# Performance work log

Hardware: AMD Instinct MI355X
Metric: run time of the kernel (lower is better)

## Reference

```python
import jax, jax.numpy as jnp
import numpy as np

B, T, C, H = 2, 2048, 1024, 16
D = C // H  # head_dim = 64


def setup_inputs() -> dict:
    key = jax.random.key(0)
    k1, k2, k3 = jax.random.split(key, 3)
    scale = 0.02
    return {
        "x": jax.random.normal(k1, (B, T, C), dtype=jnp.float32),
        "w_qkv": jax.random.normal(k2, (C, 3 * C), dtype=jnp.float32) * scale,
        "b_qkv": jnp.zeros((3 * C,), dtype=jnp.float32),
        "w_out": jax.random.normal(k3, (C, C), dtype=jnp.float32) * scale,
        "b_out": jnp.zeros((C,), dtype=jnp.float32),
    }


def reference(x, w_qkv, b_qkv, w_out, b_out):
    b, t, c = x.shape
    qkv = x @ w_qkv + b_qkv                       # [b, t, 3c]
    q, k, v = jnp.split(qkv, 3, axis=-1)
    # [b, t, c] -> [b, h, t, d]
    q = q.reshape(b, t, H, D).transpose(0, 2, 1, 3)
    k = k.reshape(b, t, H, D).transpose(0, 2, 1, 3)
    v = v.reshape(b, t, H, D).transpose(0, 2, 1, 3)
    scores = jnp.einsum("bhqd,bhkd->bhqk", q, k) / jnp.sqrt(jnp.asarray(D, dtype=q.dtype))
    causal = jnp.tril(jnp.ones((t, t), dtype=bool))
    scores = jnp.where(causal, scores, jnp.finfo(scores.dtype).min)
    attn = jax.nn.softmax(scores, axis=-1)        # [b, h, q, k]
    out = jnp.einsum("bhqk,bhkd->bhqd", attn, v)  # [b, h, t, d]
    out = out.transpose(0, 2, 1, 3).reshape(b, t, c)
    return out @ w_out + b_out
```

## Files before the change

### kernel.cpp

```cpp
#include <hip/hip_runtime.h>

#define B_ 2
#define T_ 2048
#define C_ 1024
#define H_ 16
#define D_ 64

using bf16x8 = __attribute__((ext_vector_type(8))) short;
using f32x4  = __attribute__((ext_vector_type(4))) float;

static __device__ __forceinline__ short f2bf(float f) {
  unsigned u = __builtin_bit_cast(unsigned, f);
  unsigned r = u + 0x7fffu + ((u >> 16) & 1u);
  return (short)(r >> 16);
}

#define GLD16(gp, lp) __builtin_amdgcn_global_load_lds( \
    (const __attribute__((address_space(1))) void*)(gp), \
    (__attribute__((address_space(3))) void*)(lp), 16, 0, 0)

__global__ __launch_bounds__(256) void cast_f32_bf16(const float* __restrict__ in,
                                                     short* __restrict__ out) {
  int i = blockIdx.x * blockDim.x + threadIdx.x;
  float4 v = ((const float4*)in)[i];
  short4 o;
  o.x = f2bf(v.x); o.y = f2bf(v.y); o.z = f2bf(v.z); o.w = f2bf(v.w);
  ((short4*)out)[i] = o;
}

__global__ __launch_bounds__(256) void transpose_cast(const float* __restrict__ in,
                                                      short* __restrict__ out,
                                                      int R, int N) {
  __shared__ float tile[32][33];
  int bx = blockIdx.x * 32, by = blockIdx.y * 32;
  int tx = threadIdx.x, ty = threadIdx.y;
  #pragma unroll
  for (int j = 0; j < 32; j += 8)
    tile[ty + j][tx] = in[(size_t)(by + ty + j) * N + bx + tx];
  __syncthreads();
  #pragma unroll
  for (int j = 0; j < 32; j += 8)
    out[(size_t)(bx + ty + j) * R + by + tx] = f2bf(tile[tx][ty + j]);
}

__global__ __launch_bounds__(256) void gemm_qkv(const short* __restrict__ A,
                                                const short* __restrict__ Bt,
                                                const float* __restrict__ bias,
                                                short* __restrict__ Qo,
                                                short* __restrict__ Ko,
                                                short* __restrict__ Vo) {
  __shared__ short sA[128 * 64];
  __shared__ short sB[128 * 64];
  const int tid = threadIdx.x;
  const int w = tid >> 6, lane = tid & 63;
  const int wm = w >> 1, wn = w & 1;
  const int g = lane >> 4, r16 = lane & 15;
  const int m0 = blockIdx.x * 128, n0 = blockIdx.y * 128;
  const int krow = lane >> 3, kslot = lane & 7;

  f32x4 acc[4][4] = {};

  for (int k0 = 0; k0 < 1024; k0 += 64) {
    __syncthreads();
    #pragma unroll
    for (int p = 0; p < 4; ++p) {
      int rbase = w * 32 + p * 8;
      int row = rbase + krow;
      GLD16(&A[(size_t)(m0 + row) * 1024 + k0 + ((kslot ^ (row & 7)) * 8)], &sA[rbase * 64]);
      GLD16(&Bt[(size_t)(n0 + row) * 1024 + k0 + ((kslot ^ (row & 7)) * 8)], &sB[rbase * 64]);
    }
    __syncthreads();
    bf16x8 af[4][2], bf[4][2];
    #pragma unroll
    for (int mi = 0; mi < 4; ++mi) {
      int row = wm * 64 + mi * 16 + r16;
      #pragma unroll
      for (int c = 0; c < 2; ++c)
        af[mi][c] = *(const bf16x8*)&sA[row * 64 + (((c * 4 + g) ^ (row & 7)) * 8)];
    }
    #pragma unroll
    for (int ni = 0; ni < 4; ++ni) {
      int row = wn * 64 + ni * 16 + r16;
      #pragma unroll
      for (int c = 0; c < 2; ++c)
        bf[ni][c] = *(const bf16x8*)&sB[row * 64 + (((c * 4 + g) ^ (row & 7)) * 8)];
    }
    __builtin_amdgcn_s_setprio(1);
    #pragma unroll
    for (int mi = 0; mi < 4; ++mi)
      #pragma unroll
      for (int ni = 0; ni < 4; ++ni) {
        acc[mi][ni] = __builtin_amdgcn_mfma_f32_16x16x32_bf16(af[mi][0], bf[ni][0], acc[mi][ni], 0, 0, 0);
        acc[mi][ni] = __builtin_amdgcn_mfma_f32_16x16x32_bf16(af[mi][1], bf[ni][1], acc[mi][ni], 0, 0, 0);
      }
    __builtin_amdgcn_s_setprio(0);
  }

  #pragma unroll
  for (int mi = 0; mi < 4; ++mi) {
    #pragma unroll
    for (int ni = 0; ni < 4; ++ni) {
      int n = n0 + wn * 64 + ni * 16 + r16;
      float bv = bias[n];
      int which = n >> 10;
      int c = n & 1023;
      int hh = c >> 6, d = c & 63;
      short* dst = (which == 0) ? Qo : ((which == 1) ? Ko : Vo);
      float sc = (which == 0) ? 0.18033688f : 1.0f;
      #pragma unroll
      for (int rr = 0; rr < 4; ++rr) {
        int m = m0 + wm * 64 + mi * 16 + g * 4 + rr;
        int b = m >> 11, t = m & 2047;
        dst[(size_t)((b * H_ + hh) * T_ + t) * D_ + d] = f2bf((acc[mi][ni][rr] + bv) * sc);
      }
    }
  }
}

__global__ __launch_bounds__(256) void gemm_out(const short* __restrict__ A,
                                                const short* __restrict__ Bt,
                                                const float* __restrict__ bias,
                                                float* __restrict__ Out) {
  __shared__ short sA[128 * 64];
  __shared__ short sB[128 * 64];
  const int tid = threadIdx.x;
  const int w = tid >> 6, lane = tid & 63;
  const int wm = w >> 1, wn = w & 1;
  const int g = lane >> 4, r16 = lane & 15;
  const int m0 = blockIdx.x * 128, n0 = blockIdx.y * 128;
  const int krow = lane >> 3, kslot = lane & 7;

  f32x4 acc[4][4] = {};

  for (int k0 = 0; k0 < 1024; k0 += 64) {
    __syncthreads();
    #pragma unroll
    for (int p = 0; p < 4; ++p) {
      int rbase = w * 32 + p * 8;
      int row = rbase + krow;
      GLD16(&A[(size_t)(m0 + row) * 1024 + k0 + ((kslot ^ (row & 7)) * 8)], &sA[rbase * 64]);
      GLD16(&Bt[(size_t)(n0 + row) * 1024 + k0 + ((kslot ^ (row & 7)) * 8)], &sB[rbase * 64]);
    }
    __syncthreads();
    bf16x8 af[4][2], bf[4][2];
    #pragma unroll
    for (int mi = 0; mi < 4; ++mi) {
      int row = wm * 64 + mi * 16 + r16;
      #pragma unroll
      for (int c = 0; c < 2; ++c)
        af[mi][c] = *(const bf16x8*)&sA[row * 64 + (((c * 4 + g) ^ (row & 7)) * 8)];
    }
    #pragma unroll
    for (int ni = 0; ni < 4; ++ni) {
      int row = wn * 64 + ni * 16 + r16;
      #pragma unroll
      for (int c = 0; c < 2; ++c)
        bf[ni][c] = *(const bf16x8*)&sB[row * 64 + (((c * 4 + g) ^ (row & 7)) * 8)];
    }
    __builtin_amdgcn_s_setprio(1);
    #pragma unroll
    for (int mi = 0; mi < 4; ++mi)
      #pragma unroll
      for (int ni = 0; ni < 4; ++ni) {
        acc[mi][ni] = __builtin_amdgcn_mfma_f32_16x16x32_bf16(af[mi][0], bf[ni][0], acc[mi][ni], 0, 0, 0);
        acc[mi][ni] = __builtin_amdgcn_mfma_f32_16x16x32_bf16(af[mi][1], bf[ni][1], acc[mi][ni], 0, 0, 0);
      }
    __builtin_amdgcn_s_setprio(0);
  }

  #pragma unroll
  for (int mi = 0; mi < 4; ++mi) {
    #pragma unroll
    for (int ni = 0; ni < 4; ++ni) {
      int n = n0 + wn * 64 + ni * 16 + r16;
      float bv = bias[n];
      #pragma unroll
      for (int rr = 0; rr < 4; ++rr) {
        int m = m0 + wm * 64 + mi * 16 + g * 4 + rr;
        Out[(size_t)m * 1024 + n] = acc[mi][ni][rr] + bv;
      }
    }
  }
}

__global__ __launch_bounds__(256, 4) void attn_fwd(const short* __restrict__ Q,
                                                   const short* __restrict__ K,
                                                   const short* __restrict__ V,
                                                   short* __restrict__ O) {
  __shared__ short sK[2][64 * 64];
  __shared__ short vT[2][64 * 64];

  const int tid = threadIdx.x;
  const int w = tid >> 6, lane = tid & 63;
  const int g = lane >> 4, r16 = lane & 15;
  const int bh = blockIdx.x;
  const int b = bh >> 4, hh = bh & 15;
  const int qi = 31 - (int)blockIdx.y;
  const int q0 = qi * 64;

  const short* Qh = Q + (size_t)bh * T_ * D_;
  const short* Kh = K + (size_t)bh * T_ * D_;
  const short* Vh = V + (size_t)bh * T_ * D_;

  const int krow_in_wave = lane >> 3;
  const int kslot = lane & 7;
  const int kp = tid & 31;
  const int vd0 = (tid >> 5) * 8;
  const int vchunk = (kp >> 4) * 4 + ((kp & 7) >> 1);
  const int velem  = ((kp >> 3) & 1) * 4 + 2 * (kp & 1);

  const int qrow_a = q0 + w * 16 + r16;
  bf16x8 qf[2];
  qf[0] = *(const bf16x8*)&Qh[(size_t)qrow_a * 64 + g * 8];
  qf[1] = *(const bf16x8*)&Qh[(size_t)qrow_a * 64 + 32 + g * 8];

  f32x4 o[4] = {};
  float m_ = -1e30f, l_ = 0.f;

  const int nkt = qi + 1;

  #pragma unroll
  for (int p = 0; p < 2; ++p) {
    int row = w * 16 + p * 8 + krow_in_wave;
    GLD16(&Kh[(size_t)row * 64 + ((kslot ^ (row & 7)) * 8)], &sK[0][(w * 16 + p * 8) * 64]);
  }
  {
    int4 v0 = *(const int4*)&Vh[(size_t)(2 * kp) * 64 + vd0];
    int4 v1 = *(const int4*)&Vh[(size_t)(2 * kp + 1) * 64 + vd0];
    const short* a0 = (const short*)&v0;
    const short* a1 = (const short*)&v1;
    #pragma unroll
    for (int j = 0; j < 8; ++j) {
      int d = vd0 + j;
      int val = ((int)(unsigned short)a0[j]) | (((int)(unsigned short)a1[j]) << 16);
      *(int*)&vT[0][d * 64 + ((vchunk ^ j) * 8) + velem] = val;
    }
  }
  __syncthreads();

  for (int kt = 0; kt < nkt; ++kt) {
    const int cur = kt & 1, nxt = cur ^ 1;
    const int k0 = kt * 64;
    const bool pf = (kt + 1 < nkt);

    int4 vn0, vn1;
    if (pf) {
      const int k1 = k0 + 64;
      #pragma unroll
      for (int p = 0; p < 2; ++p) {
        int row = w * 16 + p * 8 + krow_in_wave;
        GLD16(&Kh[(size_t)(k1 + row) * 64 + ((kslot ^ (row & 7)) * 8)],
              &sK[nxt][(w * 16 + p * 8) * 64]);
      }
      vn0 = *(const int4*)&Vh[(size_t)(k1 + 2 * kp) * 64 + vd0];
      vn1 = *(const int4*)&Vh[(size_t)(k1 + 2 * kp + 1) * 64 + vd0];
    }

    f32x4 s[4] = {};
    __builtin_amdgcn_s_setprio(1);
    #pragma unroll
    for (int nt = 0; nt < 4; ++nt) {
      const int row = nt * 16 + r16;
      const int sw8 = r16 & 7;
      bf16x8 kf0 = *(const bf16x8*)&sK[cur][row * 64 + ((g ^ sw8) * 8)];
      bf16x8 kf1 = *(const bf16x8*)&sK[cur][row * 64 + (((4 + g) ^ sw8) * 8)];
      s[nt] = __builtin_amdgcn_mfma_f32_16x16x32_bf16(kf0, qf[0], s[nt], 0, 0, 0);
      s[nt] = __builtin_amdgcn_mfma_f32_16x16x32_bf16(kf1, qf[1], s[nt], 0, 0, 0);
    }
    __builtin_amdgcn_s_setprio(0);

    if (kt == nkt - 1) {
      const int qrow = w * 16 + r16;
      #pragma unroll
      for (int nt = 0; nt < 4; ++nt)
        #pragma unroll
        for (int rr = 0; rr < 4; ++rr)
          if (nt * 16 + 4 * g + rr > qrow) s[nt][rr] = -1e30f;
    }
    float pmax = s[0][0];
    #pragma unroll
    for (int nt = 0; nt < 4; ++nt)
      #pragma unroll
      for (int rr = 0; rr < 4; ++rr)
        pmax = fmaxf(pmax, s[nt][rr]);
    if (!__all(pmax - m_ <= 8.0f)) {
      float rmax = fmaxf(pmax, __shfl_xor(pmax, 16));
      rmax = fmaxf(rmax, __shfl_xor(rmax, 32));
      float mn = fmaxf(m_, rmax);
      float al = __builtin_amdgcn_exp2f(m_ - mn);
      m_ = mn;
      l_ *= al;
      float av[4];
      #pragma unroll
      for (int rr = 0; rr < 4; ++rr) av[rr] = __shfl(al, 4 * g + rr, 16);
      #pragma unroll
      for (int nt = 0; nt < 4; ++nt)
        #pragma unroll
        for (int rr = 0; rr < 4; ++rr) o[nt][rr] *= av[rr];
    }
    float rs = 0.f;
    #pragma unroll
    for (int nt = 0; nt < 4; ++nt)
      #pragma unroll
      for (int rr = 0; rr < 4; ++rr) {
        float p = __builtin_amdgcn_exp2f(s[nt][rr] - m_);
        s[nt][rr] = p;
        rs += p;
      }
    l_ += rs;
    int pk[8];
    #pragma unroll
    for (int nt = 0; nt < 4; ++nt)
      #pragma unroll
      for (int h = 0; h < 2; ++h)
        asm("v_cvt_pk_bf16_f32 %0, %1, %2"
            : "=v"(pk[nt * 2 + h])
            : "v"(s[nt][2 * h]), "v"(s[nt][2 * h + 1]));

    bf16x8 pa[2];
    {
      int4 t0; t0.x = pk[0]; t0.y = pk[1]; t0.z = pk[2]; t0.w = pk[3];
      int4 t1; t1.x = pk[4]; t1.y = pk[5]; t1.z = pk[6]; t1.w = pk[7];
      pa[0] = __builtin_bit_cast(bf16x8, t0);
      pa[1] = __builtin_bit_cast(bf16x8, t1);
    }
    __builtin_amdgcn_s_setprio(1);
    #pragma unroll
    for (int nt = 0; nt < 4; ++nt) {
      const int d = nt * 16 + r16;
      bf16x8 vb0 = *(const bf16x8*)&vT[cur][d * 64 + ((g ^ (d & 7)) * 8)];
      bf16x8 vb1 = *(const bf16x8*)&vT[cur][d * 64 + (((4 + g) ^ (d & 7)) * 8)];
      o[nt] = __builtin_amdgcn_mfma_f32_16x16x32_bf16(pa[0], vb0, o[nt], 0, 0, 0);
      o[nt] = __builtin_amdgcn_mfma_f32_16x16x32_bf16(pa[1], vb1, o[nt], 0, 0, 0);
    }
    __builtin_amdgcn_s_setprio(0);

    if (pf) {
      const short* a0 = (const short*)&vn0;
      const short* a1 = (const short*)&vn1;
      #pragma unroll
      for (int j = 0; j < 8; ++j) {
        int d = vd0 + j;
        int val = ((int)(unsigned short)a0[j]) | (((int)(unsigned short)a1[j]) << 16);
        *(int*)&vT[nxt][d * 64 + ((vchunk ^ j) * 8) + velem] = val;
      }
    }
    __syncthreads();
  }

  float lt = l_ + __shfl_xor(l_, 16);
  lt += __shfl_xor(lt, 32);
  float lv[4];
  #pragma unroll
  for (int rr = 0; rr < 4; ++rr) lv[rr] = __shfl(lt, 4 * g + rr, 16);
  #pragma unroll
  for (int nt = 0; nt < 4; ++nt) {
    int d = nt * 16 + r16;
    #pragma unroll
    for (int rr = 0; rr < 4; ++rr) {
      int t = q0 + w * 16 + 4 * g + rr;
      O[(size_t)(b * T_ + t) * C_ + hh * 64 + d] = f2bf(o[nt][rr] / lv[rr]);
    }
  }
}

extern "C" void kernel_launch(void* const* d_in, const int* in_sizes, int n_in,
                              void* d_out, int out_size, void* d_ws, size_t ws_size,
                              hipStream_t stream) {
  const float* x     = (const float*)d_in[0];
  const float* w_qkv = (const float*)d_in[1];
  const float* b_qkv = (const float*)d_in[2];
  const float* w_out = (const float*)d_in[3];
  const float* b_out = (const float*)d_in[4];
  float* out = (float*)d_out;

  char* ws = (char*)d_ws;
  if (ws_size < (size_t)(40u << 20)) return;

  short* xb     = (short*)(ws);
  short* wqkvT  = (short*)(ws + ((size_t)8u << 20));
  short* woutT  = (short*)(ws + ((size_t)14u << 20));
  short* Qb     = (short*)(ws + ((size_t)16u << 20));
  short* Kb     = (short*)(ws + ((size_t)24u << 20));
  short* Vb     = (short*)(ws + ((size_t)32u << 20));
  short* attn_o = xb;

  cast_f32_bf16<<<4096, 256, 0, stream>>>(x, xb);
  transpose_cast<<<dim3(96, 32), dim3(32, 8), 0, stream>>>(w_qkv, wqkvT, 1024, 3072);
  transpose_cast<<<dim3(32, 32), dim3(32, 8), 0, stream>>>(w_out, woutT, 1024, 1024);
  gemm_qkv<<<dim3(32, 24), 256, 0, stream>>>(xb, wqkvT, b_qkv, Qb, Kb, Vb);
  attn_fwd<<<dim3(32, 32), 256, 0, stream>>>(Qb, Kb, Vb, attn_o);
  gemm_out<<<dim3(32, 8), 256, 0, stream>>>(attn_o, woutT, b_out, out);
}
```

Before: 119.3 us.

## Software-pipeline PV matmul one tile behind QK with triple-buffered V

The P·V MFMA for tile kt-1 now runs at the start of iteration kt, before the QK^T MFMAs and softmax of tile kt. This lets matrix work overlap with the exponent and reduction work within a wave. V staging in LDS grows from two to three buffers so the deferred tile stays valid, and an epilogue after the loop handles the last tile. The row max and row sum reductions are also rewritten as balanced trees to shorten dependency chains. The extra V buffer raises LDS use per block, which could limit occupancy.

```diff
diff --git a/kernel.cpp b/kernel.cpp
--- a/kernel.cpp
+++ b/kernel.cpp
@@ -188,7 +188,7 @@
                                                    const short* __restrict__ V,
                                                    short* __restrict__ O) {
   __shared__ short sK[2][64 * 64];
-  __shared__ short vT[2][64 * 64];
+  __shared__ short vT[3][64 * 64];
 
   const int tid = threadIdx.x;
   const int w = tid >> 6, lane = tid & 63;
@@ -216,6 +216,7 @@
 
   f32x4 o[4] = {};
   float m_ = -1e30f, l_ = 0.f;
+  bf16x8 pa[2];
 
   const int nkt = qi + 1;
 
@@ -254,6 +255,20 @@
       }
       vn0 = *(const int4*)&Vh[(size_t)(k1 + 2 * kp) * 64 + vd0];
       vn1 = *(const int4*)&Vh[(size_t)(k1 + 2 * kp + 1) * 64 + vd0];
+    }
+
+    if (kt > 0) {
+      const short* vp = vT[(kt - 1) % 3];
+      __builtin_amdgcn_s_setprio(1);
+      #pragma unroll
+      for (int nt = 0; nt < 4; ++nt) {
+        const int d = nt * 16 + r16;
+        bf16x8 vb0 = *(const bf16x8*)&vp[d * 64 + ((g ^ (d & 7)) * 8)];
+        bf16x8 vb1 = *(const bf16x8*)&vp[d * 64 + (((4 + g) ^ (d & 7)) * 8)];
+        o[nt] = __builtin_amdgcn_mfma_f32_16x16x32_bf16(pa[0], vb0, o[nt], 0, 0, 0);
+        o[nt] = __builtin_amdgcn_mfma_f32_16x16x32_bf16(pa[1], vb1, o[nt], 0, 0, 0);
+      }
+      __builtin_amdgcn_s_setprio(0);
     }
 
     f32x4 s[4] = {};
@@ -277,12 +292,13 @@
         for (int rr = 0; rr < 4; ++rr)
           if (nt * 16 + 4 * g + rr > qrow) s[nt][rr] = -1e30f;
     }
-    float pmax = s[0][0];
-    #pragma unroll
-    for (int nt = 0; nt < 4; ++nt)
-      #pragma unroll
-      for (int rr = 0; rr < 4; ++rr)
-        pmax = fmaxf(pmax, s[nt][rr]);
+    float x0 = fmaxf(s[0][0], s[0][1]), x1 = fmaxf(s[0][2], s[0][3]);
+    float x2 = fmaxf(s[1][0], s[1][1]), x3 = fmaxf(s[1][2], s[1][3]);
+    float x4 = fmaxf(s[2][0], s[2][1]), x5 = fmaxf(s[2][2], s[2][3]);
+    float x6 = fmaxf(s[3][0], s[3][1]), x7 = fmaxf(s[3][2], s[3][3]);
+    x0 = fmaxf(x0, x1); x2 = fmaxf(x2, x3); x4 = fmaxf(x4, x5); x6 = fmaxf(x6, x7);
+    x0 = fmaxf(x0, x2); x4 = fmaxf(x4, x6);
+    float pmax = fmaxf(x0, x4);
     if (!__all(pmax - m_ <= 8.0f)) {
       float rmax = fmaxf(pmax, __shfl_xor(pmax, 16));
       rmax = fmaxf(rmax, __shfl_xor(rmax, 32));
@@ -298,16 +314,18 @@
         #pragma unroll
         for (int rr = 0; rr < 4; ++rr) o[nt][rr] *= av[rr];
     }
-    float rs = 0.f;
     #pragma unroll
     for (int nt = 0; nt < 4; ++nt)
       #pragma unroll
-      for (int rr = 0; rr < 4; ++rr) {
-        float p = __builtin_amdgcn_exp2f(s[nt][rr] - m_);
-        s[nt][rr] = p;
-        rs += p;
-      }
-    l_ += rs;
+      for (int rr = 0; rr < 4; ++rr)
+        s[nt][rr] = __builtin_amdgcn_exp2f(s[nt][rr] - m_);
+    float y0 = s[0][0] + s[0][1], y1 = s[0][2] + s[0][3];
+    float y2 = s[1][0] + s[1][1], y3 = s[1][2] + s[1][3];
+    float y4 = s[2][0] + s[2][1], y5 = s[2][2] + s[2][3];
+    float y6 = s[3][0] + s[3][1], y7 = s[3][2] + s[3][3];
+    y0 += y1; y2 += y3; y4 += y5; y6 += y7;
+    y0 += y2; y4 += y6;
+    l_ += y0 + y4;
     int pk[8];
     #pragma unroll
     for (int nt = 0; nt < 4; ++nt)
@@ -316,36 +334,37 @@
         asm("v_cvt_pk_bf16_f32 %0, %1, %2"
             : "=v"(pk[nt * 2 + h])
             : "v"(s[nt][2 * h]), "v"(s[nt][2 * h + 1]));
-
-    bf16x8 pa[2];
     {
       int4 t0; t0.x = pk[0]; t0.y = pk[1]; t0.z = pk[2]; t0.w = pk[3];
       int4 t1; t1.x = pk[4]; t1.y = pk[5]; t1.z = pk[6]; t1.w = pk[7];
       pa[0] = __builtin_bit_cast(bf16x8, t0);
       pa[1] = __builtin_bit_cast(bf16x8, t1);
     }
-    __builtin_amdgcn_s_setprio(1);
-    #pragma unroll
-    for (int nt = 0; nt < 4; ++nt) {
-      const int d = nt * 16 + r16;
-      bf16x8 vb0 = *(const bf16x8*)&vT[cur][d * 64 + ((g ^ (d & 7)) * 8)];
-      bf16x8 vb1 = *(const bf16x8*)&vT[cur][d * 64 + (((4 + g) ^ (d & 7)) * 8)];
-      o[nt] = __builtin_amdgcn_mfma_f32_16x16x32_bf16(pa[0], vb0, o[nt], 0, 0, 0);
-      o[nt] = __builtin_amdgcn_mfma_f32_16x16x32_bf16(pa[1], vb1, o[nt], 0, 0, 0);
-    }
-    __builtin_amdgcn_s_setprio(0);
 
     if (pf) {
+      short* vpn = vT[(kt + 1) % 3];
       const short* a0 = (const short*)&vn0;
       const short* a1 = (const short*)&vn1;
       #pragma unroll
       for (int j = 0; j < 8; ++j) {
         int d = vd0 + j;
         int val = ((int)(unsigned short)a0[j]) | (((int)(unsigned short)a1[j]) << 16);
-        *(int*)&vT[nxt][d * 64 + ((vchunk ^ j) * 8) + velem] = val;
+        *(int*)&vpn[d * 64 + ((vchunk ^ j) * 8) + velem] = val;
       }
     }
     __syncthreads();
+  }
+
+  {
+    const short* vp = vT[(nkt - 1) % 3];
+    #pragma unroll
+    for (int nt = 0; nt < 4; ++nt) {
+      const int d = nt * 16 + r16;
+      bf16x8 vb0 = *(const bf16x8*)&vp[d * 64 + ((g ^ (d & 7)) * 8)];
+      bf16x8 vb1 = *(const bf16x8*)&vp[d * 64 + (((4 + g) ^ (d & 7)) * 8)];
+      o[nt] = __builtin_amdgcn_mfma_f32_16x16x32_bf16(pa[0], vb0, o[nt], 0, 0, 0);
+      o[nt] = __builtin_amdgcn_mfma_f32_16x16x32_bf16(pa[1], vb1, o[nt], 0, 0, 0);
+    }
   }
 
   float lt = l_ + __shfl_xor(l_, 16);
```

Measured after the change: 119.3 us. About the same (-0.0%).

## Give attention waves two query subtiles each and narrow the output GEMM tile

Applied to the files above, without the earlier changes.

The attention kernel now runs 2 waves per block instead of 4. Each wave handles 32 query rows as two 16-row subtiles, so every K and V fragment read from LDS feeds twice as many MFMAs. K/V tile loading is redistributed so the smaller block still fills the full 64x64 tiles. The output projection GEMM uses 128x64 tiles, doubling its grid from 256 to 512 blocks for better CU coverage. The trade-offs are fewer resident waves per CU in attention, higher register pressure, and less B-operand reuse in the GEMM.

```diff
diff --git a/kernel.cpp b/kernel.cpp
--- a/kernel.cpp
+++ b/kernel.cpp
@@ -122,15 +122,15 @@
                                                 const float* __restrict__ bias,
                                                 float* __restrict__ Out) {
   __shared__ short sA[128 * 64];
-  __shared__ short sB[128 * 64];
+  __shared__ short sB[64 * 64];
   const int tid = threadIdx.x;
   const int w = tid >> 6, lane = tid & 63;
   const int wm = w >> 1, wn = w & 1;
   const int g = lane >> 4, r16 = lane & 15;
-  const int m0 = blockIdx.x * 128, n0 = blockIdx.y * 128;
+  const int m0 = blockIdx.x * 128, n0 = blockIdx.y * 64;
   const int krow = lane >> 3, kslot = lane & 7;
 
-  f32x4 acc[4][4] = {};
+  f32x4 acc[4][2] = {};
 
   for (int k0 = 0; k0 < 1024; k0 += 64) {
     __syncthreads();
@@ -139,10 +139,15 @@
       int rbase = w * 32 + p * 8;
       int row = rbase + krow;
       GLD16(&A[(size_t)(m0 + row) * 1024 + k0 + ((kslot ^ (row & 7)) * 8)], &sA[rbase * 64]);
+    }
+    #pragma unroll
+    for (int p = 0; p < 2; ++p) {
+      int rbase = w * 16 + p * 8;
+      int row = rbase + krow;
       GLD16(&Bt[(size_t)(n0 + row) * 1024 + k0 + ((kslot ^ (row & 7)) * 8)], &sB[rbase * 64]);
     }
     __syncthreads();
-    bf16x8 af[4][2], bf[4][2];
+    bf16x8 af[4][2], bf[2][2];
     #pragma unroll
     for (int mi = 0; mi < 4; ++mi) {
       int row = wm * 64 + mi * 16 + r16;
@@ -151,8 +156,8 @@
         af[mi][c] = *(const bf16x8*)&sA[row * 64 + (((c * 4 + g) ^ (row & 7)) * 8)];
     }
     #pragma unroll
-    for (int ni = 0; ni < 4; ++ni) {
-      int row = wn * 64 + ni * 16 + r16;
+    for (int ni = 0; ni < 2; ++ni) {
+      int row = wn * 32 + ni * 16 + r16;
       #pragma unroll
       for (int c = 0; c < 2; ++c)
         bf[ni][c] = *(const bf16x8*)&sB[row * 64 + (((c * 4 + g) ^ (row & 7)) * 8)];
@@ -161,7 +166,7 @@
     #pragma unroll
     for (int mi = 0; mi < 4; ++mi)
       #pragma unroll
-      for (int ni = 0; ni < 4; ++ni) {
+      for (int ni = 0; ni < 2; ++ni) {
         acc[mi][ni] = __builtin_amdgcn_mfma_f32_16x16x32_bf16(af[mi][0], bf[ni][0], acc[mi][ni], 0, 0, 0);
         acc[mi][ni] = __builtin_amdgcn_mfma_f32_16x16x32_bf16(af[mi][1], bf[ni][1], acc[mi][ni], 0, 0, 0);
       }
@@ -171,8 +176,8 @@
   #pragma unroll
   for (int mi = 0; mi < 4; ++mi) {
     #pragma unroll
-    for (int ni = 0; ni < 4; ++ni) {
-      int n = n0 + wn * 64 + ni * 16 + r16;
+    for (int ni = 0; ni < 2; ++ni) {
+      int n = n0 + wn * 32 + ni * 16 + r16;
       float bv = bias[n];
       #pragma unroll
       for (int rr = 0; rr < 4; ++rr) {
@@ -183,7 +188,7 @@
   }
 }
 
-__global__ __launch_bounds__(256, 4) void attn_fwd(const short* __restrict__ Q,
+__global__ __launch_bounds__(128, 2) void attn_fwd(const short* __restrict__ Q,
                                                    const short* __restrict__ K,
                                                    const short* __restrict__ V,
                                                    short* __restrict__ O) {
@@ -202,38 +207,44 @@
   const short* Kh = K + (size_t)bh * T_ * D_;
   const short* Vh = V + (size_t)bh * T_ * D_;
 
-  const int krow_in_wave = lane >> 3;
-  const int kslot = lane & 7;
+  const int krw = lane >> 3, kslot = lane & 7;
   const int kp = tid & 31;
   const int vd0 = (tid >> 5) * 8;
   const int vchunk = (kp >> 4) * 4 + ((kp & 7) >> 1);
   const int velem  = ((kp >> 3) & 1) * 4 + 2 * (kp & 1);
 
-  const int qrow_a = q0 + w * 16 + r16;
-  bf16x8 qf[2];
-  qf[0] = *(const bf16x8*)&Qh[(size_t)qrow_a * 64 + g * 8];
-  qf[1] = *(const bf16x8*)&Qh[(size_t)qrow_a * 64 + 32 + g * 8];
-
-  f32x4 o[4] = {};
-  float m_ = -1e30f, l_ = 0.f;
+  bf16x8 qf[2][2];
+  #pragma unroll
+  for (int u = 0; u < 2; ++u) {
+    const size_t qoff = (size_t)(q0 + w * 32 + u * 16 + r16) * 64;
+    qf[u][0] = *(const bf16x8*)&Qh[qoff + g * 8];
+    qf[u][1] = *(const bf16x8*)&Qh[qoff + 32 + g * 8];
+  }
+
+  f32x4 o[2][4] = {};
+  float m_[2] = {-1e30f, -1e30f}, l_[2] = {0.f, 0.f};
 
   const int nkt = qi + 1;
 
   #pragma unroll
-  for (int p = 0; p < 2; ++p) {
-    int row = w * 16 + p * 8 + krow_in_wave;
-    GLD16(&Kh[(size_t)row * 64 + ((kslot ^ (row & 7)) * 8)], &sK[0][(w * 16 + p * 8) * 64]);
+  for (int p = 0; p < 4; ++p) {
+    int row = w * 32 + p * 8 + krw;
+    GLD16(&Kh[(size_t)row * 64 + ((kslot ^ (row & 7)) * 8)], &sK[0][(w * 32 + p * 8) * 64]);
   }
   {
-    int4 v0 = *(const int4*)&Vh[(size_t)(2 * kp) * 64 + vd0];
-    int4 v1 = *(const int4*)&Vh[(size_t)(2 * kp + 1) * 64 + vd0];
-    const short* a0 = (const short*)&v0;
-    const short* a1 = (const short*)&v1;
+    int4 va0 = *(const int4*)&Vh[(size_t)(2 * kp) * 64 + vd0];
+    int4 va1 = *(const int4*)&Vh[(size_t)(2 * kp + 1) * 64 + vd0];
+    int4 vb0_ = *(const int4*)&Vh[(size_t)(2 * kp) * 64 + vd0 + 32];
+    int4 vb1_ = *(const int4*)&Vh[(size_t)(2 * kp + 1) * 64 + vd0 + 32];
+    const short* a0 = (const short*)&va0; const short* a1 = (const short*)&va1;
+    const short* b0 = (const short*)&vb0_; const short* b1 = (const short*)&vb1_;
     #pragma unroll
     for (int j = 0; j < 8; ++j) {
       int d = vd0 + j;
-      int val = ((int)(unsigned short)a0[j]) | (((int)(unsigned short)a1[j]) << 16);
-      *(int*)&vT[0][d * 64 + ((vchunk ^ j) * 8) + velem] = val;
+      int lo = ((int)(unsigned short)a0[j]) | (((int)(unsigned short)a1[j]) << 16);
+      int hi2 = ((int)(unsigned short)b0[j]) | (((int)(unsigned short)b1[j]) << 16);
+      *(int*)&vT[0][d * 64 + ((vchunk ^ j) * 8) + velem] = lo;
+      *(int*)&vT[0][(d + 32) * 64 + ((vchunk ^ j) * 8) + velem] = hi2;
     }
   }
   __syncthreads();
@@ -243,20 +254,22 @@
     const int k0 = kt * 64;
     const bool pf = (kt + 1 < nkt);
 
-    int4 vn0, vn1;
+    int4 va0, va1, vb0_, vb1_;
     if (pf) {
       const int k1 = k0 + 64;
       #pragma unroll
-      for (int p = 0; p < 2; ++p) {
-        int row = w * 16 + p * 8 + krow_in_wave;
+      for (int p = 0; p < 4; ++p) {
+        int row = w * 32 + p * 8 + krw;
         GLD16(&Kh[(size_t)(k1 + row) * 64 + ((kslot ^ (row & 7)) * 8)],
-              &sK[nxt][(w * 16 + p * 8) * 64]);
-      }
-      vn0 = *(const int4*)&Vh[(size_t)(k1 + 2 * kp) * 64 + vd0];
-      vn1 = *(const int4*)&Vh[(size_t)(k1 + 2 * kp + 1) * 64 + vd0];
-    }
-
-    f32x4 s[4] = {};
+              &sK[nxt][(w * 32 + p * 8) * 64]);
+      }
+      va0 = *(const int4*)&Vh[(size_t)(k1 + 2 * kp) * 64 + vd0];
+      va1 = *(const int4*)&Vh[(size_t)(k1 + 2 * kp + 1) * 64 + vd0];
+      vb0_ = *(const int4*)&Vh[(size_t)(k1 + 2 * kp) * 64 + vd0 + 32];
+      vb1_ = *(const int4*)&Vh[(size_t)(k1 + 2 * kp + 1) * 64 + vd0 + 32];
+    }
+
+    f32x4 s[2][4] = {};
     __builtin_amdgcn_s_setprio(1);
     #pragma unroll
     for (int nt = 0; nt < 4; ++nt) {
@@ -264,102 +277,112 @@
       const int sw8 = r16 & 7;
       bf16x8 kf0 = *(const bf16x8*)&sK[cur][row * 64 + ((g ^ sw8) * 8)];
       bf16x8 kf1 = *(const bf16x8*)&sK[cur][row * 64 + (((4 + g) ^ sw8) * 8)];
-      s[nt] = __builtin_amdgcn_mfma_f32_16x16x32_bf16(kf0, qf[0], s[nt], 0, 0, 0);
-      s[nt] = __builtin_amdgcn_mfma_f32_16x16x32_bf16(kf1, qf[1], s[nt], 0, 0, 0);
+      s[0][nt] = __builtin_amdgcn_mfma_f32_16x16x32_bf16(kf0, qf[0][0], s[0][nt], 0, 0, 0);
+      s[0][nt] = __builtin_amdgcn_mfma_f32_16x16x32_bf16(kf1, qf[0][1], s[0][nt], 0, 0, 0);
+      s[1][nt] = __builtin_amdgcn_mfma_f32_16x16x32_bf16(kf0, qf[1][0], s[1][nt], 0, 0, 0);
+      s[1][nt] = __builtin_amdgcn_mfma_f32_16x16x32_bf16(kf1, qf[1][1], s[1][nt], 0, 0, 0);
     }
     __builtin_amdgcn_s_setprio(0);
 
-    if (kt == nkt - 1) {
-      const int qrow = w * 16 + r16;
+    bf16x8 pa[2][2];
+    #pragma unroll
+    for (int u = 0; u < 2; ++u) {
+      if (kt == nkt - 1) {
+        const int qrow = w * 32 + u * 16 + r16;
+        #pragma unroll
+        for (int nt = 0; nt < 4; ++nt)
+          #pragma unroll
+          for (int rr = 0; rr < 4; ++rr)
+            if (nt * 16 + 4 * g + rr > qrow) s[u][nt][rr] = -1e30f;
+      }
+      float pmax = s[u][0][0];
       #pragma unroll
       for (int nt = 0; nt < 4; ++nt)
         #pragma unroll
         for (int rr = 0; rr < 4; ++rr)
-          if (nt * 16 + 4 * g + rr > qrow) s[nt][rr] = -1e30f;
-    }
-    float pmax = s[0][0];
-    #pragma unroll
-    for (int nt = 0; nt < 4; ++nt)
-      #pragma unroll
-      for (int rr = 0; rr < 4; ++rr)
-        pmax = fmaxf(pmax, s[nt][rr]);
-    if (!__all(pmax - m_ <= 8.0f)) {
-      float rmax = fmaxf(pmax, __shfl_xor(pmax, 16));
-      rmax = fmaxf(rmax, __shfl_xor(rmax, 32));
-      float mn = fmaxf(m_, rmax);
-      float al = __builtin_amdgcn_exp2f(m_ - mn);
-      m_ = mn;
-      l_ *= al;
-      float av[4];
-      #pragma unroll
-      for (int rr = 0; rr < 4; ++rr) av[rr] = __shfl(al, 4 * g + rr, 16);
+          pmax = fmaxf(pmax, s[u][nt][rr]);
+      if (!__all(pmax - m_[u] <= 8.0f)) {
+        float rmax = fmaxf(pmax, __shfl_xor(pmax, 16));
+        rmax = fmaxf(rmax, __shfl_xor(rmax, 32));
+        float mn = fmaxf(m_[u], rmax);
+        float al = __builtin_amdgcn_exp2f(m_[u] - mn);
+        m_[u] = mn;
+        l_[u] *= al;
+        float av[4];
+        #pragma unroll
+        for (int rr = 0; rr < 4; ++rr) av[rr] = __shfl(al, 4 * g + rr, 16);
+        #pragma unroll
+        for (int nt = 0; nt < 4; ++nt)
+          #pragma unroll
+          for (int rr = 0; rr < 4; ++rr) o[u][nt][rr] *= av[rr];
+      }
+      float rs = 0.f;
       #pragma unroll
       for (int nt = 0; nt < 4; ++nt)
         #pragma unroll
-        for (int rr = 0; rr < 4; ++rr) o[nt][rr] *= av[rr];
-    }
-    float rs = 0.f;
-    #pragma unroll
-    for (int nt = 0; nt < 4; ++nt)
-      #pragma unroll
-      for (int rr = 0; rr < 4; ++rr) {
-        float p = __builtin_amdgcn_exp2f(s[nt][rr] - m_);
-        s[nt][rr] = p;
-        rs += p;
-      }
-    l_ += rs;
-    int pk[8];
-    #pragma unroll
-    for (int nt = 0; nt < 4; ++nt)
-      #pragma unroll
-      for (int h = 0; h < 2; ++h)
-        asm("v_cvt_pk_bf16_f32 %0, %1, %2"
-            : "=v"(pk[nt * 2 + h])
-            : "v"(s[nt][2 * h]), "v"(s[nt][2 * h + 1]));
-
-    bf16x8 pa[2];
-    {
+        for (int rr = 0; rr < 4; ++rr) {
+          float p = __builtin_amdgcn_exp2f(s[u][nt][rr] - m_[u]);
+          s[u][nt][rr] = p;
+          rs += p;
+        }
+      l_[u] += rs;
+      int pk[8];
+      #pragma unroll
+      for (int nt = 0; nt < 4; ++nt)
+        #pragma unroll
+        for (int h = 0; h < 2; ++h)
+          asm("v_cvt_pk_bf16_f32 %0, %1, %2"
+              : "=v"(pk[nt * 2 + h])
+              : "v"(s[u][nt][2 * h]), "v"(s[u][nt][2 * h + 1]));
       int4 t0; t0.x = pk[0]; t0.y = pk[1]; t0.z = pk[2]; t0.w = pk[3];
       int4 t1; t1.x = pk[4]; t1.y = pk[5]; t1.z = pk[6]; t1.w = pk[7];
-      pa[0] = __builtin_bit_cast(bf16x8, t0);
-      pa[1] = __builtin_bit_cast(bf16x8, t1);
-    }
+      pa[u][0] = __builtin_bit_cast(bf16x8, t0);
+      pa[u][1] = __builtin_bit_cast(bf16x8, t1);
+    }
+
     __builtin_amdgcn_s_setprio(1);
     #pragma unroll
     for (int nt = 0; nt < 4; ++nt) {
       const int d = nt * 16 + r16;
       bf16x8 vb0 = *(const bf16x8*)&vT[cur][d * 64 + ((g ^ (d & 7)) * 8)];
       bf16x8 vb1 = *(const bf16x8*)&vT[cur][d * 64 + (((4 + g) ^ (d & 7)) * 8)];
-      o[nt] = __builtin_amdgcn_mfma_f32_16x16x32_bf16(pa[0], vb0, o[nt], 0, 0, 0);
-      o[nt] = __builtin_amdgcn_mfma_f32_16x16x32_bf16(pa[1], vb1, o[nt], 0, 0, 0);
+      o[0][nt] = __builtin_amdgcn_mfma_f32_16x16x32_bf16(pa[0][0], vb0, o[0][nt], 0, 0, 0);
+      o[0][nt] = __builtin_amdgcn_mfma_f32_16x16x32_bf16(pa[0][1], vb1, o[0][nt], 0, 0, 0);
+      o[1][nt] = __builtin_amdgcn_mfma_f32_16x16x32_bf16(pa[1][0], vb0, o[1][nt], 0, 0, 0);
+      o[1][nt] = __builtin_amdgcn_mfma_f32_16x16x32_bf16(pa[1][1], vb1, o[1][nt], 0, 0, 0);
     }
     __builtin_amdgcn_s_setprio(0);
 
     if (pf) {
-      const short* a0 = (const short*)&vn0;
-      const short* a1 = (const short*)&vn1;
+      const short* a0 = (const short*)&va0; const short* a1 = (const short*)&va1;
+      const short* b0 = (const short*)&vb0_; const short* b1 = (const short*)&vb1_;
       #pragma unroll
       for (int j = 0; j < 8; ++j) {
         int d = vd0 + j;
-        int val = ((int)(unsigned short)a0[j]) | (((int)(unsigned short)a1[j]) << 16);
-        *(int*)&vT[nxt][d * 64 + ((vchunk ^ j) * 8) + velem] = val;
+        int lo = ((int)(unsigned short)a0[j]) | (((int)(unsigned short)a1[j]) << 16);
+        int hi2 = ((int)(unsigned short)b0[j]) | (((int)(unsigned short)b1[j]) << 16);
+        *(int*)&vT[nxt][d * 64 + ((vchunk ^ j) * 8) + velem] = lo;
+        *(int*)&vT[nxt][(d + 32) * 64 + ((vchunk ^ j) * 8) + velem] = hi2;
       }
     }
     __syncthreads();
   }
 
-  float lt = l_ + __shfl_xor(l_, 16);
-  lt += __shfl_xor(lt, 32);
-  float lv[4];
-  #pragma unroll
-  for (int rr = 0; rr < 4; ++rr) lv[rr] = __shfl(lt, 4 * g + rr, 16);
-  #pragma unroll
-  for (int nt = 0; nt < 4; ++nt) {
-    int d = nt * 16 + r16;
-    #pragma unroll
-    for (int rr = 0; rr < 4; ++rr) {
-      int t = q0 + w * 16 + 4 * g + rr;
-      O[(size_t)(b * T_ + t) * C_ + hh * 64 + d] = f2bf(o[nt][rr] / lv[rr]);
+  #pragma unroll
+  for (int u = 0; u < 2; ++u) {
+    float lt = l_[u] + __shfl_xor(l_[u], 16);
+    lt += __shfl_xor(lt, 32);
+    float lv[4];
+    #pragma unroll
+    for (int rr = 0; rr < 4; ++rr) lv[rr] = __shfl(lt, 4 * g + rr, 16);
+    #pragma unroll
+    for (int nt = 0; nt < 4; ++nt) {
+      int d = nt * 16 + r16;
+      #pragma unroll
+      for (int rr = 0; rr < 4; ++rr) {
+        int t = q0 + w * 32 + u * 16 + 4 * g + rr;
+        O[(size_t)(b * T_ + t) * C_ + hh * 64 + d] = f2bf(o[u][nt][rr] / lv[rr]);
+      }
     }
   }
 }
@@ -389,6 +412,6 @@
   transpose_cast<<<dim3(96, 32), dim3(32, 8), 0, stream>>>(w_qkv, wqkvT, 1024, 3072);
   transpose_cast<<<dim3(32, 32), dim3(32, 8), 0, stream>>>(w_out, woutT, 1024, 1024);
   gemm_qkv<<<dim3(32, 24), 256, 0, stream>>>(xb, wqkvT, b_qkv, Qb, Kb, Vb);
-  attn_fwd<<<dim3(32, 32), 256, 0, stream>>>(Qb, Kb, Vb, attn_o);
-  gemm_out<<<dim3(32, 8), 256, 0, stream>>>(attn_o, woutT, b_out, out);
-}
+  attn_fwd<<<dim3(32, 32), 128, 0, stream>>>(Qb, Kb, Vb, attn_o);
+  gemm_out<<<dim3(32, 16), 256, 0, stream>>>(attn_o, woutT, b_out, out);
+}
```

New measurement: 126.3 us. +5.8%, slower.
